# Kernel optimization log

Measured on AMD Instinct MI355X. Metric: run time of the kernel, lower is better.

The kernel has to match this reference:

```python
import jax, jax.numpy as jnp
import numpy as np
from jax import lax

WINDOW_SIZE = 11
CHANNEL = 3
SIGMA = 1.5


def _build_window():
    # 1D gaussian, normalized, then outer product -> (C, 1, k, k) depthwise kernel
    coords = jnp.arange(WINDOW_SIZE, dtype=jnp.float32) - WINDOW_SIZE // 2
    g = jnp.exp(-coords ** 2 / (2.0 * SIGMA ** 2))
    g = g / g.sum()
    w2d = jnp.outer(g, g)  # (k, k)
    return jnp.broadcast_to(w2d[None, None], (CHANNEL, 1, WINDOW_SIZE, WINDOW_SIZE))


def _dwconv(x, w):
    pad = WINDOW_SIZE // 2
    return lax.conv_general_dilated(
        x, w,
        window_strides=(1, 1),
        padding=[(pad, pad), (pad, pad)],
        dimension_numbers=("NCHW", "OIHW", "NCHW"),
        feature_group_count=CHANNEL,
    )


def setup_inputs() -> dict:
    key = jax.random.key(0)
    k1, k2 = jax.random.split(key)
    pred = jax.random.uniform(k1, (16, 3, 512, 512), dtype=jnp.float32)
    target = jax.random.uniform(k2, (16, 3, 512, 512), dtype=jnp.float32)
    return {"pred": pred, "target": target}


def reference(pred, target):
    C1, C2 = 0.01 ** 2, 0.03 ** 2
    w = _build_window().astype(pred.dtype)

    mu_x = _dwconv(pred, w)
    mu_y = _dwconv(target, w)
    mu_x_sq = mu_x * mu_x
    mu_y_sq = mu_y * mu_y
    mu_xy = mu_x * mu_y

    sg_x = _dwconv(pred * pred, w) - mu_x_sq
    sg_y = _dwconv(target * target, w) - mu_y_sq
    sg_xy = _dwconv(pred * target, w) - mu_xy

    ssim_map = ((2.0 * mu_xy + C1) * (2.0 * sg_xy + C2)) / (
        (mu_x_sq + mu_y_sq + C1) * (sg_x + sg_y + C2)
    )
    return 1.0 - ssim_map.mean()
```

## Files before the change

kernel.cpp:

```cpp
#include <hip/hip_runtime.h>


namespace {
constexpr int IMG   = 512;
constexpr int NCH   = 48;
constexpr int TPX   = IMG / 16;
constexpr int NTILE = TPX * TPX * NCH;
constexpr int NBLK  = NTILE / 4;
constexpr int RS    = 40;

constexpr float Wf[11] = {
    0.00102838f, 0.00759876f, 0.03600077f, 0.10936069f, 0.21300554f,
    0.26601172f,
    0.21300554f, 0.10936069f, 0.03600077f, 0.00759876f, 0.00102838f };

constexpr float band_wc(int d) {
    return (d >= 0 && d < 11) ? Wf[d] : 0.f;
}

constexpr unsigned short f2h(float f) {
    if (f == 0.f) return 0;
    unsigned u = __builtin_bit_cast(unsigned, f);
    int  he = int((u >> 23) & 0xff) - 127 + 15;
    unsigned hm   = (u & 0x7fffff) >> 13;
    unsigned rest = u & 0x1fff;
    if (rest > 0x1000 || (rest == 0x1000 && (hm & 1))) ++hm;
    return (unsigned short)((unsigned(he) << 10) + hm);
}

struct Tabs { unsigned short a[64][8]; unsigned short b[64][8]; };
constexpr Tabs build_tabs() {
    Tabs t{};
    for (int lane = 0; lane < 64; ++lane) {
        const int nr = lane & 15, quad = lane >> 4;
        for (int jj = 0; jj < 8; ++jj) {
            const int k = quad * 8 + jj;
            t.a[lane][jj] = f2h(band_wc(k - nr));
            t.b[lane][jj] = f2h(band_wc(k - nr - 3));
        }
    }
    return t;
}
}

__device__ __constant__ __align__(16) Tabs g_tabs = build_tabs();

typedef _Float16 half8 __attribute__((ext_vector_type(8)));
typedef _Float16 half4v __attribute__((ext_vector_type(4)));
typedef _Float16 h2 __attribute__((ext_vector_type(2)));
typedef float float4v __attribute__((ext_vector_type(4)));
typedef float float2v __attribute__((ext_vector_type(2)));

__device__ inline h2 pk(float a, float b) {
    auto v = __builtin_amdgcn_cvt_pkrtz(a, b);
    h2 r;
    __builtin_memcpy(&r, &v, sizeof(r));
    return r;
}

union H8 { half8 v; h2 p[4]; };

__global__ __launch_bounds__(256, 6) void ssim_fused_kernel(
    const float* __restrict__ pred, const float* __restrict__ tgt,
    float* __restrict__ partial)
{
    __shared__ __align__(16) _Float16 hf[4][2][16][RS];

    const int t    = threadIdx.x;
    const int w    = t >> 6;
    const int lane = t & 63;
    const int nr   = lane & 15;
    const int quad = lane >> 4;

    const int tid  = blockIdx.x * 4 + w;
    const int img  = tid >> 10;
    const int tile = tid & 1023;
    const int tx   = (tile & 31) * 16;
    const int ty   = (tile >> 5) * 16;

    const float* __restrict__ p = pred + (size_t)img * (IMG * IMG);
    const float* __restrict__ q = tgt  + (size_t)img * (IMG * IMG);

    const half8 Aband = *(const half8*)(g_tabs.a[lane]);
    const half8 Bband = *(const half8*)(g_tabs.b[lane]);
    const float4v zf = {0.f, 0.f, 0.f, 0.f};
    const half8 z8 = {};

    const int cb  = tx - 8 + (quad << 3);
    const int cbc = min(max(cb, 0), IMG - 8);
    const bool okc = ((unsigned)cb <= (unsigned)(IMG - 8));

    float4 xa[2], xb[2], ya[2], yb[2];
    bool ok[2];
    #pragma unroll
    for (int s = 0; s < 2; ++s) {
        const int gy  = ty + 16 * s + nr - 5;
        const int gyc = min(max(gy, 0), IMG - 1);
        ok[s] = ((unsigned)gy < (unsigned)IMG) && okc;
        const float* rp = p + gyc * IMG + cbc;
        const float* rq = q + gyc * IMG + cbc;
        xa[s] = *(const float4*)rp;
        xb[s] = *(const float4*)(rp + 4);
        ya[s] = *(const float4*)rq;
        yb[s] = *(const float4*)(rq + 4);
    }

    half8 fx[2], fy[2];
    #pragma unroll
    for (int s = 0; s < 2; ++s) {
        H8 ax, ay;
        ax.p[0] = pk(xa[s].x, xa[s].y); ax.p[1] = pk(xa[s].z, xa[s].w);
        ax.p[2] = pk(xb[s].x, xb[s].y); ax.p[3] = pk(xb[s].z, xb[s].w);
        ay.p[0] = pk(ya[s].x, ya[s].y); ay.p[1] = pk(ya[s].z, ya[s].w);
        ay.p[2] = pk(yb[s].x, yb[s].y); ay.p[3] = pk(yb[s].z, yb[s].w);
        if (!ok[s]) { ax.v = z8; ay.v = z8; }
        fx[s] = ax.v;
        fy[s] = ay.v;
    }

    const int wr = quad << 2;
    auto hwrite = [&](int slot, int s, float4v d) {
        h2 lo = pk(d[0], d[1]);
        h2 hi = pk(d[2], d[3]);
        half4v hh = {lo[0], lo[1], hi[0], hi[1]};
        *(half4v*)&hf[w][slot][nr][16 * s + wr] = hh;
    };
    auto hread = [&](int slot) -> half8 {
        return *(const half8*)&hf[w][slot][nr][quad << 3];
    };
    auto HM = [&](half8 a) {
        return __builtin_amdgcn_mfma_f32_16x16x32_f16(a, Bband, zf, 0, 0, 0);
    };
    auto VM = [&](half8 b) {
        return __builtin_amdgcn_mfma_f32_16x16x32_f16(Aband, b, zf, 0, 0, 0);
    };

    float4v acc[5];
    hwrite(0, 0, HM(fx[0]));  hwrite(0, 1, HM(fx[1]));
    hwrite(1, 0, HM(fy[0]));  hwrite(1, 1, HM(fy[1]));
    acc[0] = VM(hread(0));
    acc[1] = VM(hread(1));
    hwrite(0, 0, HM(fx[0] * fx[0]));  hwrite(0, 1, HM(fx[1] * fx[1]));
    hwrite(1, 0, HM(fy[0] * fy[0]));  hwrite(1, 1, HM(fy[1] * fy[1]));
    acc[2] = VM(hread(0));
    acc[3] = VM(hread(1));
    hwrite(0, 0, HM(fx[0] * fy[0]));  hwrite(0, 1, HM(fx[1] * fy[1]));
    acc[4] = VM(hread(0));

    constexpr float C1 = 1e-4f, C2 = 9e-4f;
    const float2v C1v = {C1, C1};
    const float2v C2v = {C2, C2};
    const float2v K12 = {C1 + C2, C1 + C2};
    float2v lsum2 = {0.f, 0.f};
    #pragma unroll
    for (int h = 0; h < 2; ++h) {
        float2v mx  = {acc[0][2*h], acc[0][2*h+1]};
        float2v my  = {acc[1][2*h], acc[1][2*h+1]};
        float2v ex2 = {acc[2][2*h], acc[2][2*h+1]};
        float2v ey2 = {acc[3][2*h], acc[3][2*h+1]};
        float2v exy = {acc[4][2*h], acc[4][2*h+1]};
        float2v P  = mx * my;
        float2v U  = mx * mx + my * my + C1v;
        float2v n1 = 2.f * P + C1v;
        float2v n2 = 2.f * (exy - P) + C2v;
        float2v num = n1 * n2;
        float2v e1 = (ex2 + ey2) - U + K12;
        float2v den = U * e1;
        float2v r = {__builtin_amdgcn_rcpf(den.x),
                     __builtin_amdgcn_rcpf(den.y)};
        lsum2 += num * r;
    }
    float lsum = lsum2.x + lsum2.y;

    #pragma unroll
    for (int off = 32; off > 0; off >>= 1)
        lsum += __shfl_down(lsum, off, 64);
    if (lane == 0) partial[tid] = lsum;
}

__global__ __launch_bounds__(1024) void ssim_finish(
    const float* __restrict__ partial, float* __restrict__ out)
{
    __shared__ float wred[16];
    const int t = threadIdx.x;
    float s = 0.f;
    #pragma unroll
    for (int i = 0; i < NTILE / 1024; ++i)
        s += partial[t + i * 1024];
    #pragma unroll
    for (int off = 32; off > 0; off >>= 1)
        s += __shfl_down(s, off, 64);
    if ((t & 63) == 0) wred[t >> 6] = s;
    __syncthreads();
    if (t == 0) {
        float acc = 0.f;
        #pragma unroll
        for (int i = 0; i < 16; ++i) acc += wred[i];
        out[0] = 1.f - acc * (1.f / (float)((long long)NCH * IMG * IMG));
    }
}

extern "C" void kernel_launch(void* const* d_in, const int* in_sizes, int n_in,
                              void* d_out, int out_size, void* d_ws, size_t ws_size,
                              hipStream_t stream)
{
    const float* pred = (const float*)d_in[0];
    const float* tgt  = (const float*)d_in[1];
    float* out     = (float*)d_out;
    float* partial = (float*)d_ws;

    ssim_fused_kernel<<<NBLK, 256, 0, stream>>>(pred, tgt, partial);
    ssim_finish<<<1, 1024, 0, stream>>>(partial, out);
}
```

Measured before the change: 146.7 us.

## Stage 128x32 input tiles in LDS via direct global-to-LDS loads

Each block now covers a 128x32 output tile and first copies the haloed input window for both images into LDS with global_load_lds, using a swizzled slot layout to limit bank conflicts. Each wave then processes two 16-column strips of 32 rows, with three 16-row MFMA input blocks per strip. Before, every wave loaded its own 16x16 tile's halo straight from global memory, so halo data was fetched many times over. Reuse rises, but the kernel needs about 50KB of LDS per block, cutting occupancy to 2 blocks per CU, and the single up-front load followed by a barrier leaves memory latency largely exposed.

Result: faster. 130.0 us (-11.4%).

```diff
diff --git a/kernel.cpp b/kernel.cpp
--- a/kernel.cpp
+++ b/kernel.cpp
@@ -4,10 +4,19 @@
 namespace {
 constexpr int IMG   = 512;
 constexpr int NCH   = 48;
-constexpr int TPX   = IMG / 16;
-constexpr int NTILE = TPX * TPX * NCH;
-constexpr int NBLK  = NTILE / 4;
-constexpr int RS    = 40;
+constexpr int TW    = 128;
+constexpr int TH    = 32;
+constexpr int WR    = 44;
+constexpr int WC    = 144;
+constexpr int SLOTS = WC / 4;
+constexpr int TSLOT = WR * SLOTS;
+constexpr int NLDI  = 50;
+constexpr int TPX   = IMG / TW;
+constexpr int TPY   = IMG / TH;
+constexpr int NBLK  = TPX * TPY * NCH;
+constexpr int NPART = NBLK * 4;
+constexpr int RS    = 56;
+constexpr int SXN   = WR * WC;
 
 constexpr float Wf[11] = {
     0.00102838f, 0.00759876f, 0.03600077f, 0.10936069f, 0.21300554f,
@@ -60,11 +69,18 @@
 
 union H8 { half8 v; h2 p[4]; };
 
-__global__ __launch_bounds__(256, 6) void ssim_fused_kernel(
+__device__ __forceinline__ void gl2l(const float* g, void* l) {
+    __builtin_amdgcn_global_load_lds(
+        (const __attribute__((address_space(1))) unsigned int*)g,
+        (__attribute__((address_space(3))) unsigned int*)l, 16, 0, 0);
+}
+
+__global__ __launch_bounds__(256, 2) void ssim_tile_kernel(
     const float* __restrict__ pred, const float* __restrict__ tgt,
     float* __restrict__ partial)
 {
-    __shared__ __align__(16) _Float16 hf[4][2][16][RS];
+    __shared__ __align__(16) float sx[2 * SXN];
+    __shared__ __align__(16) _Float16 sc[4][2][16][RS];
 
     const int t    = threadIdx.x;
     const int w    = t >> 6;
@@ -72,110 +88,136 @@
     const int nr   = lane & 15;
     const int quad = lane >> 4;
 
-    const int tid  = blockIdx.x * 4 + w;
-    const int img  = tid >> 10;
-    const int tile = tid & 1023;
-    const int tx   = (tile & 31) * 16;
-    const int ty   = (tile >> 5) * 16;
+    const int bid  = blockIdx.x;
+    const int img  = bid >> 6;
+    const int tile = bid & 63;
+    const int tx   = (tile & 3) * TW;
+    const int ty   = (tile >> 2) * TH;
 
     const float* __restrict__ p = pred + (size_t)img * (IMG * IMG);
     const float* __restrict__ q = tgt  + (size_t)img * (IMG * IMG);
+
+    #pragma unroll
+    for (int i = 0; i < 13; ++i) {
+        const int j = i * 4 + w;
+        if (j < NLDI) {
+            const int L = j * 64 + lane;
+            if (L < 2 * TSLOT) {
+                const int tens = (L >= TSLOT) ? 1 : 0;
+                const int Lt   = L - tens * TSLOT;
+                const int row  = Lt / SLOTS;
+                const int sp   = Lt - row * SLOTS;
+                int sl = sp - (row & 7);
+                if (sl < 0) sl += SLOTS;
+                const int gy   = min(max(ty - 5 + row, 0), IMG - 1);
+                const int gx   = min(max(tx - 8 + 4 * sl, 0), IMG - 4);
+                const float* src = (tens ? q : p) + gy * IMG + gx;
+                gl2l(src, (char*)sx + (size_t)j * 1024);
+            }
+        }
+    }
+    __syncthreads();
 
     const half8 Aband = *(const half8*)(g_tabs.a[lane]);
     const half8 Bband = *(const half8*)(g_tabs.b[lane]);
     const float4v zf = {0.f, 0.f, 0.f, 0.f};
     const half8 z8 = {};
-
-    const int cb  = tx - 8 + (quad << 3);
-    const int cbc = min(max(cb, 0), IMG - 8);
-    const bool okc = ((unsigned)cb <= (unsigned)(IMG - 8));
-
-    float4 xa[2], xb[2], ya[2], yb[2];
-    bool ok[2];
-    #pragma unroll
-    for (int s = 0; s < 2; ++s) {
-        const int gy  = ty + 16 * s + nr - 5;
-        const int gyc = min(max(gy, 0), IMG - 1);
-        ok[s] = ((unsigned)gy < (unsigned)IMG) && okc;
-        const float* rp = p + gyc * IMG + cbc;
-        const float* rq = q + gyc * IMG + cbc;
-        xa[s] = *(const float4*)rp;
-        xb[s] = *(const float4*)(rp + 4);
-        ya[s] = *(const float4*)rq;
-        yb[s] = *(const float4*)(rq + 4);
-    }
-
-    half8 fx[2], fy[2];
-    #pragma unroll
-    for (int s = 0; s < 2; ++s) {
-        H8 ax, ay;
-        ax.p[0] = pk(xa[s].x, xa[s].y); ax.p[1] = pk(xa[s].z, xa[s].w);
-        ax.p[2] = pk(xb[s].x, xb[s].y); ax.p[3] = pk(xb[s].z, xb[s].w);
-        ay.p[0] = pk(ya[s].x, ya[s].y); ay.p[1] = pk(ya[s].z, ya[s].w);
-        ay.p[2] = pk(yb[s].x, yb[s].y); ay.p[3] = pk(yb[s].z, yb[s].w);
-        if (!ok[s]) { ax.v = z8; ay.v = z8; }
-        fx[s] = ax.v;
-        fy[s] = ay.v;
-    }
-
-    const int wr = quad << 2;
-    auto hwrite = [&](int slot, int s, float4v d) {
-        h2 lo = pk(d[0], d[1]);
-        h2 hi = pk(d[2], d[3]);
-        half4v hh = {lo[0], lo[1], hi[0], hi[1]};
-        *(half4v*)&hf[w][slot][nr][16 * s + wr] = hh;
-    };
-    auto hread = [&](int slot) -> half8 {
-        return *(const half8*)&hf[w][slot][nr][quad << 3];
-    };
-    auto HM = [&](half8 a) {
-        return __builtin_amdgcn_mfma_f32_16x16x32_f16(a, Bband, zf, 0, 0, 0);
-    };
-    auto VM = [&](half8 b) {
-        return __builtin_amdgcn_mfma_f32_16x16x32_f16(Aband, b, zf, 0, 0, 0);
-    };
-
-    float4v acc[5];
-    hwrite(0, 0, HM(fx[0]));  hwrite(0, 1, HM(fx[1]));
-    hwrite(1, 0, HM(fy[0]));  hwrite(1, 1, HM(fy[1]));
-    acc[0] = VM(hread(0));
-    acc[1] = VM(hread(1));
-    hwrite(0, 0, HM(fx[0] * fx[0]));  hwrite(0, 1, HM(fx[1] * fx[1]));
-    hwrite(1, 0, HM(fy[0] * fy[0]));  hwrite(1, 1, HM(fy[1] * fy[1]));
-    acc[2] = VM(hread(0));
-    acc[3] = VM(hread(1));
-    hwrite(0, 0, HM(fx[0] * fy[0]));  hwrite(0, 1, HM(fx[1] * fy[1]));
-    acc[4] = VM(hread(0));
 
     constexpr float C1 = 1e-4f, C2 = 9e-4f;
     const float2v C1v = {C1, C1};
     const float2v C2v = {C2, C2};
     const float2v K12 = {C1 + C2, C1 + C2};
     float2v lsum2 = {0.f, 0.f};
-    #pragma unroll
-    for (int h = 0; h < 2; ++h) {
-        float2v mx  = {acc[0][2*h], acc[0][2*h+1]};
-        float2v my  = {acc[1][2*h], acc[1][2*h+1]};
-        float2v ex2 = {acc[2][2*h], acc[2][2*h+1]};
-        float2v ey2 = {acc[3][2*h], acc[3][2*h+1]};
-        float2v exy = {acc[4][2*h], acc[4][2*h+1]};
-        float2v P  = mx * my;
-        float2v U  = mx * mx + my * my + C1v;
-        float2v n1 = 2.f * P + C1v;
-        float2v n2 = 2.f * (exy - P) + C2v;
-        float2v num = n1 * n2;
-        float2v e1 = (ex2 + ey2) - U + K12;
-        float2v den = U * e1;
-        float2v r = {__builtin_amdgcn_rcpf(den.x),
-                     __builtin_amdgcn_rcpf(den.y)};
-        lsum2 += num * r;
-    }
+
+    #pragma unroll 1
+    for (int cc = 0; cc < 2; ++cc) {
+        const int c = w + 4 * cc;
+        const bool okc_ = ((unsigned)(tx + 16 * c - 8 + 8 * quad)
+                           <= (unsigned)(IMG - 8));
+
+        half8 fx[3], fy[3];
+        #pragma unroll
+        for (int s = 0; s < 3; ++s) {
+            const int row  = 16 * s + nr;
+            const int rowr = min(row, WR - 1);
+            const bool ok  = okc_ && (row < WR) &&
+                             ((unsigned)(ty - 5 + row) < (unsigned)IMG);
+            const int sl0 = 4 * c + 2 * quad;
+            const int r7  = rowr & 7;
+            int pos0 = sl0 + r7;     if (pos0 >= SLOTS) pos0 -= SLOTS;
+            int pos1 = sl0 + 1 + r7; if (pos1 >= SLOTS) pos1 -= SLOTS;
+            const float* b0 = sx + rowr * WC;
+            const float* b1 = b0 + SXN;
+            float4 xA = *(const float4*)(b0 + 4 * pos0);
+            float4 xB = *(const float4*)(b0 + 4 * pos1);
+            float4 yA = *(const float4*)(b1 + 4 * pos0);
+            float4 yB = *(const float4*)(b1 + 4 * pos1);
+            H8 ax, ay;
+            ax.p[0] = pk(xA.x, xA.y); ax.p[1] = pk(xA.z, xA.w);
+            ax.p[2] = pk(xB.x, xB.y); ax.p[3] = pk(xB.z, xB.w);
+            ay.p[0] = pk(yA.x, yA.y); ay.p[1] = pk(yA.z, yA.w);
+            ay.p[2] = pk(yB.x, yB.y); ay.p[3] = pk(yB.z, yB.w);
+            if (!ok) { ax.v = z8; ay.v = z8; }
+            fx[s] = ax.v;
+            fy[s] = ay.v;
+        }
+
+        auto hw = [&](int slot, int s, float4v d) {
+            h2 lo = pk(d[0], d[1]);
+            h2 hi = pk(d[2], d[3]);
+            half4v hh = {lo[0], lo[1], hi[0], hi[1]};
+            *(half4v*)&sc[w][slot][nr][16 * s + 4 * quad] = hh;
+        };
+        auto rdv = [&](int slot, int pb) -> half8 {
+            return *(const half8*)&sc[w][slot][nr][pb + 8 * quad];
+        };
+        #define HMA(a) __builtin_amdgcn_mfma_f32_16x16x32_f16((a), Bband, zf, 0, 0, 0)
+        #define VMA(b) __builtin_amdgcn_mfma_f32_16x16x32_f16(Aband, (b), zf, 0, 0, 0)
+
+        float4v a0[5], a1[5];
+        #pragma unroll
+        for (int s = 0; s < 3; ++s) { hw(0, s, HMA(fx[s])); hw(1, s, HMA(fy[s])); }
+        a0[0] = VMA(rdv(0, 0));  a1[0] = VMA(rdv(0, 16));
+        a0[1] = VMA(rdv(1, 0));  a1[1] = VMA(rdv(1, 16));
+        #pragma unroll
+        for (int s = 0; s < 3; ++s) { hw(0, s, HMA(fx[s] * fx[s])); hw(1, s, HMA(fy[s] * fy[s])); }
+        a0[2] = VMA(rdv(0, 0));  a1[2] = VMA(rdv(0, 16));
+        a0[3] = VMA(rdv(1, 0));  a1[3] = VMA(rdv(1, 16));
+        #pragma unroll
+        for (int s = 0; s < 3; ++s) { hw(0, s, HMA(fx[s] * fy[s])); }
+        a0[4] = VMA(rdv(0, 0));  a1[4] = VMA(rdv(0, 16));
+
+        #pragma unroll
+        for (int v = 0; v < 2; ++v) {
+            const float4v* A = v ? a1 : a0;
+            #pragma unroll
+            for (int h = 0; h < 2; ++h) {
+                float2v mx  = {A[0][2*h], A[0][2*h+1]};
+                float2v my  = {A[1][2*h], A[1][2*h+1]};
+                float2v ex2 = {A[2][2*h], A[2][2*h+1]};
+                float2v ey2 = {A[3][2*h], A[3][2*h+1]};
+                float2v exy = {A[4][2*h], A[4][2*h+1]};
+                float2v P  = mx * my;
+                float2v U  = mx * mx + my * my + C1v;
+                float2v n1 = 2.f * P + C1v;
+                float2v n2 = 2.f * (exy - P) + C2v;
+                float2v num = n1 * n2;
+                float2v e1 = (ex2 + ey2) - U + K12;
+                float2v den = U * e1;
+                float2v r = {__builtin_amdgcn_rcpf(den.x),
+                             __builtin_amdgcn_rcpf(den.y)};
+                lsum2 += num * r;
+            }
+        }
+        #undef HMA
+        #undef VMA
+    }
+
     float lsum = lsum2.x + lsum2.y;
-
     #pragma unroll
     for (int off = 32; off > 0; off >>= 1)
         lsum += __shfl_down(lsum, off, 64);
-    if (lane == 0) partial[tid] = lsum;
+    if (lane == 0) partial[(bid << 2) + w] = lsum;
 }
 
 __global__ __launch_bounds__(1024) void ssim_finish(
@@ -185,7 +227,7 @@
     const int t = threadIdx.x;
     float s = 0.f;
     #pragma unroll
-    for (int i = 0; i < NTILE / 1024; ++i)
+    for (int i = 0; i < NPART / 1024; ++i)
         s += partial[t + i * 1024];
     #pragma unroll
     for (int off = 32; off > 0; off >>= 1)
@@ -209,6 +251,6 @@
     float* out     = (float*)d_out;
     float* partial = (float*)d_ws;
 
-    ssim_fused_kernel<<<NBLK, 256, 0, stream>>>(pred, tgt, partial);
+    ssim_tile_kernel<<<NBLK, 256, 0, stream>>>(pred, tgt, partial);
     ssim_finish<<<1, 1024, 0, stream>>>(partial, out);
 }
```
